# Kernel optimization log

Measured on AMD Instinct MI355X. Metric: run time of the kernel, lower is better.

## Reference

```python
import jax, jax.numpy as jnp
import numpy as np


def _lstm1_step(x, Wih, bih, bhh):
    # nn.LSTM applied to a length-1 sequence with zero initial (h, c):
    # h_prev = 0 so W_hh contributes 0; c = sigmoid(i)*tanh(g); h = sigmoid(o)*tanh(c).
    gates = x @ Wih.T + bih + bhh            # (..., 4H), torch gate order i,f,g,o
    i, f, g, o = jnp.split(gates, 4, axis=-1)
    c = jax.nn.sigmoid(i) * jnp.tanh(g)
    return jax.nn.sigmoid(o) * jnp.tanh(c)


def _lstm2_layer(x, Wih, Whh, bih, bhh):
    # Full recurrent LSTM layer over time; x: (B, T, H) -> outputs (B, T, H).
    B = x.shape[0]
    H = Whh.shape[1]
    xg = x @ Wih.T + bih + bhh               # precompute input gates (B, T, 4H)
    def step(carry, g_t):                    # g_t: (B, 4H)
        h, c = carry
        gates = g_t + h @ Whh.T
        i, f, g, o = jnp.split(gates, 4, axis=-1)
        c = jax.nn.sigmoid(f) * c + jax.nn.sigmoid(i) * jnp.tanh(g)
        h = jax.nn.sigmoid(o) * jnp.tanh(c)
        return (h, c), h
    h0 = jnp.zeros((B, H), x.dtype)
    _, hs = jax.lax.scan(step, (h0, h0), jnp.swapaxes(xg, 0, 1))
    return jnp.swapaxes(hs, 0, 1)            # (B, T, H)


def setup_inputs() -> dict:
    D, H, B, T = 256, 1024, 64, 256
    key = jax.random.key(0)
    ks = iter(jax.random.split(key, 32))
    s = 1.0 / np.sqrt(H).astype(np.float32)
    def u(shape):
        return jax.random.uniform(next(ks), shape, jnp.float32, -s, s)
    inp = {"xx": jax.random.normal(next(ks), (B, T, D), jnp.float32)}
    inp.update(
        l1_Wih0=u((4 * H, D)), l1_bih0=u((4 * H,)), l1_bhh0=u((4 * H,)),
        l1_Wih1=u((4 * H, H)), l1_bih1=u((4 * H,)), l1_bhh1=u((4 * H,)),
        l2_Wih0=u((4 * H, H)), l2_Whh0=u((4 * H, H)), l2_bih0=u((4 * H,)), l2_bhh0=u((4 * H,)),
        l2_Wih1=u((4 * H, H)), l2_Whh1=u((4 * H, H)), l2_bih1=u((4 * H,)), l2_bhh1=u((4 * H,)),
        mlp_W1=u((H, H)), mlp_b1=u((H,)),
        mlp_W2=u((H // 2, H)), mlp_b2=u((H // 2,)),
        mlp_W3=u((1, H // 2)), mlp_b3=u((1,)),
    )
    return inp


def reference(xx, l1_Wih0, l1_bih0, l1_bhh0, l1_Wih1, l1_bih1, l1_bhh1,
              l2_Wih0, l2_Whh0, l2_bih0, l2_bhh0, l2_Wih1, l2_Whh1, l2_bih1, l2_bhh1,
              mlp_W1, mlp_b1, mlp_W2, mlp_b2, mlp_W3, mlp_b3):
    # lstm1: per-timestep single-step stacked LSTM cell with zero state (vectorized over B,T)
    h = _lstm1_step(xx, l1_Wih0, l1_bih0, l1_bhh0)
    h = _lstm1_step(h, l1_Wih1, l1_bih1, l1_bhh1)          # (B, T, H) == lsout
    # lstm2: true 2-layer recurrence over T
    h = _lstm2_layer(h, l2_Wih0, l2_Whh0, l2_bih0, l2_bhh0)
    h = _lstm2_layer(h, l2_Wih1, l2_Whh1, l2_bih1, l2_bhh1)
    last = h[:, -1, :]                                     # (B, H)
    z = jax.nn.relu(last @ mlp_W1.T + mlp_b1)
    z = jax.nn.relu(z @ mlp_W2.T + mlp_b2)
    out = z @ mlp_W3.T + mlp_b3                            # (B, 1)
    return out[:, 0]                                       # out_m: (B,)
```

## Files before the change

### kernel.cpp

```cpp
#include <hip/hip_runtime.h>

typedef unsigned short u16;
typedef unsigned int u32;
typedef u16 u16x8 __attribute__((ext_vector_type(8)));
typedef u16 u16x4 __attribute__((ext_vector_type(4)));
typedef __bf16 bf16x8 __attribute__((ext_vector_type(8)));
typedef float f32x4 __attribute__((ext_vector_type(4)));

#define B_ 64
#define T_ 256
#define D_ 256
#define H_ 1024
#define G4 4096
#define TC 64
#define MC 4096
#define NCHUNK 4
#define NFLG 2048

__device__ __forceinline__ u16 f2bf(float x) {
  u32 u = __builtin_bit_cast(u32, x);
  u += 0x7fffu + ((u >> 16) & 1u);
  return (u16)(u >> 16);
}
__device__ __forceinline__ float bf2f(u16 h) {
  u32 u = ((u32)h) << 16;
  return __builtin_bit_cast(float, u);
}
__device__ __forceinline__ float sigmoidf_(float x) { return 1.f / (1.f + __expf(-x)); }

__device__ __forceinline__ f32x4 mfma16(u16x8 a, u16x8 b, f32x4 c) {
  return __builtin_amdgcn_mfma_f32_16x16x32_bf16(
      __builtin_bit_cast(bf16x8, a), __builtin_bit_cast(bf16x8, b), c, 0, 0, 0);
}

__device__ __forceinline__ void gl2lds16(const u16* g, u16* l) {
  __builtin_amdgcn_global_load_lds(
      (const __attribute__((address_space(1))) u32*)(const void*)g,
      (__attribute__((address_space(3))) u32*)(void*)l, 16, 0, 0);
}

__device__ __forceinline__ void store4_cc(u16* p, u32 v) {
  asm volatile("global_store_dword %0, %1, off sc0 sc1" :: "v"(p), "v"(v) : "memory");
}
__device__ __forceinline__ void store4_cc_u32(u32* p, u32 v) {
  asm volatile("global_store_dword %0, %1, off sc0 sc1" :: "v"(p), "v"(v) : "memory");
}
__device__ __forceinline__ void waitcnt0() {
  asm volatile("s_waitcnt vmcnt(0)" ::: "memory");
}

__global__ void k_split(const float* __restrict__ src, u16* __restrict__ hi,
                        u16* __restrict__ lo, int n4) {
  int i = blockIdx.x * 256 + threadIdx.x;
  if (i >= n4) return;
  const float4* s4 = (const float4*)src;
  float4 v = s4[i];
  u16 h0 = f2bf(v.x), h1 = f2bf(v.y), h2 = f2bf(v.z), h3 = f2bf(v.w);
  u16x4 hv = {h0, h1, h2, h3};
  u16x4 lv = {f2bf(v.x - bf2f(h0)), f2bf(v.y - bf2f(h1)),
              f2bf(v.z - bf2f(h2)), f2bf(v.w - bf2f(h3))};
  *(u16x4*)(hi + 4 * (size_t)i) = hv;
  *(u16x4*)(lo + 4 * (size_t)i) = lv;
}

__global__ void k_split_x(const float* __restrict__ xx, u16* __restrict__ hi,
                          u16* __restrict__ lo, int t0) {
  int i = blockIdx.x * 256 + threadIdx.x;
  if (i >= MC * (D_ / 4)) return;
  int row = i >> 6, c4 = i & 63;
  int b = row >> 6, tc = row & 63;
  const float4* s4 = (const float4*)xx;
  float4 v = s4[(size_t)(b * T_ + t0 + tc) * (D_ / 4) + c4];
  u16 h0 = f2bf(v.x), h1 = f2bf(v.y), h2 = f2bf(v.z), h3 = f2bf(v.w);
  u16x4 hv = {h0, h1, h2, h3};
  u16x4 lv = {f2bf(v.x - bf2f(h0)), f2bf(v.y - bf2f(h1)),
              f2bf(v.z - bf2f(h2)), f2bf(v.w - bf2f(h3))};
  *(u16x4*)(hi + 4 * (size_t)i) = hv;
  *(u16x4*)(lo + 4 * (size_t)i) = lv;
}

__global__ void k_addvec(const float* __restrict__ a, const float* __restrict__ b,
                         float* __restrict__ o, int n) {
  int i = blockIdx.x * 256 + threadIdx.x;
  if (i < n) o[i] = a[i] + b[i];
}

__global__ __launch_bounds__(256, 2) void k_gemm3(
    const u16* __restrict__ Ah, const u16* __restrict__ Al,
    const u16* __restrict__ Bh, const u16* __restrict__ Bl,
    const float* __restrict__ bias, float* __restrict__ C,
    int M, int N, int K, int rec)
{
  __shared__ __attribute__((aligned(16))) u16 sAh[2][4096];
  __shared__ __attribute__((aligned(16))) u16 sAl[2][4096];
  __shared__ __attribute__((aligned(16))) u16 sBh[2][4096];
  __shared__ __attribute__((aligned(16))) u16 sBl[2][4096];

  const int tid = threadIdx.x;
  const int lane = tid & 63;
  const int wv = tid >> 6;
  const int wm = wv & 1, wn = wv >> 1;
  const int m0 = blockIdx.x * 128;
  const int n0 = blockIdx.y * 128;

  const int r0 = tid >> 2;
  const int kg = (tid & 3) ^ (r0 & 3);
  const size_t aoff0 = (size_t)(m0 + r0) * K + kg * 8;
  const size_t aoff1 = (size_t)(m0 + r0 + 64) * K + kg * 8;
  const size_t boff0 = (size_t)(n0 + r0) * K + kg * 8;
  const size_t boff1 = (size_t)(n0 + r0 + 64) * K + kg * 8;
  const int lb0 = wv * 512;
  const int lb1 = 2048 + wv * 512;

  const int l15 = lane & 15, l4 = lane >> 4;
  int afo[4], bfo[4];
#pragma unroll
  for (int mt = 0; mt < 4; ++mt) {
    int r = wm * 64 + mt * 16 + l15;
    afo[mt] = (r * 4 + (l4 ^ (r & 3))) * 8;
  }
#pragma unroll
  for (int nt = 0; nt < 4; ++nt) {
    int r = wn * 64 + nt * 16 + l15;
    bfo[nt] = (r * 4 + (l4 ^ (r & 3))) * 8;
  }

#define STAGE_G(bi, kk) do { \
    gl2lds16(Ah + aoff0 + (kk), &sAh[bi][lb0]); \
    gl2lds16(Ah + aoff1 + (kk), &sAh[bi][lb1]); \
    gl2lds16(Al + aoff0 + (kk), &sAl[bi][lb0]); \
    gl2lds16(Al + aoff1 + (kk), &sAl[bi][lb1]); \
    gl2lds16(Bh + boff0 + (kk), &sBh[bi][lb0]); \
    gl2lds16(Bh + boff1 + (kk), &sBh[bi][lb1]); \
    gl2lds16(Bl + boff0 + (kk), &sBl[bi][lb0]); \
    gl2lds16(Bl + boff1 + (kk), &sBl[bi][lb1]); \
  } while (0)

  f32x4 acc[4][4] = {};

  STAGE_G(0, 0);
  __syncthreads();

  int cur = 0;
  for (int k0 = 0; k0 < K; k0 += 32) {
    if (k0 + 32 < K) STAGE_G(cur ^ 1, k0 + 32);

    u16x8 a_h[4], a_l[4], b_h[4], b_l[4];
#pragma unroll
    for (int i = 0; i < 4; ++i) {
      a_h[i] = *(const u16x8*)&sAh[cur][afo[i]];
      a_l[i] = *(const u16x8*)&sAl[cur][afo[i]];
      b_h[i] = *(const u16x8*)&sBh[cur][bfo[i]];
      b_l[i] = *(const u16x8*)&sBl[cur][bfo[i]];
    }
#pragma unroll
    for (int mt = 0; mt < 4; ++mt)
#pragma unroll
      for (int nt = 0; nt < 4; ++nt) {
        acc[mt][nt] = mfma16(a_h[mt], b_h[nt], acc[mt][nt]);
        acc[mt][nt] = mfma16(a_l[mt], b_h[nt], acc[mt][nt]);
        acc[mt][nt] = mfma16(a_h[mt], b_l[nt], acc[mt][nt]);
      }

    __syncthreads();
    cur ^= 1;
  }
#undef STAGE_G

  if (!rec) {
#pragma unroll
    for (int mt = 0; mt < 4; ++mt) {
      int mr = m0 + wm * 64 + mt * 16 + l4 * 4;
#pragma unroll
      for (int nt = 0; nt < 4; ++nt) {
        int nc = n0 + wn * 64 + nt * 16 + l15;
        float bv = bias[nc];
#pragma unroll
        for (int r = 0; r < 4; ++r)
          C[(size_t)(mr + r) * N + nc] = acc[mt][nt][r] + bv;
      }
    }
  } else {
#pragma unroll
    for (int mt = 0; mt < 4; ++mt) {
      int mr = m0 + wm * 64 + mt * 16 + l4 * 4;
#pragma unroll
      for (int nt = 0; nt < 4; ++nt) {
        int nc = n0 + wn * 64 + nt * 16 + l15;
        float bv = bias[nc];
        int unit = nc & 1023;
        int ublk = unit >> 3;
        int uu = unit & 7;
        int gate = nc >> 10;
#pragma unroll
        for (int r = 0; r < 4; ++r) {
          int m = mr + r;
          int tq = (rec == 1) ? (m & 63) : (m >> 6);
          int bq = (rec == 1) ? (m >> 6) : (m & 63);
          size_t idx = ((size_t)(ublk * 64 + tq) * 4 + gate) * 512 + bq * 8 + uu;
          C[idx] = acc[mt][nt][r] + bv;
        }
      }
    }
  }
}

__global__ void k_pw(const float* __restrict__ xg, u16* __restrict__ hhi,
                     u16* __restrict__ hlo) {
  int idx = blockIdx.x * 256 + threadIdx.x;
  int r = idx >> 10, j = idx & 1023;
  const float* g = xg + (size_t)r * G4;
  float cc = sigmoidf_(g[j]) * tanhf(g[2048 + j]);
  float h = sigmoidf_(g[3072 + j]) * tanhf(cc);
  u16 hh = f2bf(h);
  hhi[idx] = hh;
  hlo[idx] = f2bf(h - bf2f(hh));
}

__global__ __launch_bounds__(512, 2) void k_recd(
    const float* __restrict__ xgA, const float* __restrict__ xgB,
    const u16* __restrict__ WAhi, const u16* __restrict__ WAlo,
    const u16* __restrict__ WBhi, const u16* __restrict__ WBlo,
    u16* __restrict__ rAH, u16* __restrict__ rAL,
    u16* __restrict__ rBH, u16* __restrict__ rBL,
    u16* __restrict__ cAH, u16* __restrict__ cAL,
    u16* __restrict__ cBH, u16* __restrict__ cBL,
    float* __restrict__ cbA, float* __restrict__ cbB,
    float* __restrict__ hfB,
    u32* __restrict__ flags)
{
  __shared__ __attribute__((aligned(16))) u16 sW[66048];
  __shared__ float sg[2][64][34];
  __shared__ int sDead;

  const int tid = threadIdx.x;
  const int lane = tid & 63, wv = tid >> 6;
  const int l15 = lane & 15, l4 = lane >> 4;
  const int L = blockIdx.x >> 7, ublk = blockIdx.x & 127;
  const int u0 = ublk * 8;

  const float* xg = L ? xgB : xgA;
  if (!xg) return;
  const u16* Whi = L ? WBhi : WAhi;
  const u16* Wlo = L ? WBlo : WAlo;
  u16* ringH = L ? rBH : rAH;
  u16* ringL = L ? rBL : rAL;
  u16* carryH = L ? cBH : cAH;
  u16* carryL = L ? cBL : cAL;
  float* cbp = L ? cbB : cbA;
  float* hfinal = L ? hfB : nullptr;
  u32* flg = flags + L * 1024;

  if (tid == 0) sDead = 0;

  for (int ci = tid; ci < 8192; ci += 512) {
    int plane = ci >> 12, rem = ci & 4095;
    int n = rem >> 7, ch = rem & 127;
    int wrow = (n >> 3) * 1024 + u0 + (n & 7);
    const u16* src = (plane ? Wlo : Whi) + (size_t)wrow * 1024 + ch * 8;
    *(u16x8*)&sW[plane * 33024 + n * 1032 + ch * 8] = *(const u16x8*)src;
  }
  __syncthreads();

  const int mt = wv >> 1, kh = wv & 1;
  const int aoff = (mt * 16 + l15) * 1024 + kh * 512 + l4 * 8;
  const int bof0 = l15 * 1032 + kh * 512 + l4 * 8;
  const int bof1 = (16 + l15) * 1032 + kh * 512 + l4 * 8;

  const u32* f0a = flg + (2 * mt) * 128 + kh * 64 + lane;
  const u32* f0b = flg + (2 * mt + 1) * 128 + kh * 64 + lane;
  u32* fown = flg + wv * 128 + ublk;

  const int pb = tid >> 3, uu = tid & 7;
  const int cidx = pb * 1024 + u0 + uu;
  float c = cbp[cidx];
  const float* xgb = xg + (size_t)ublk * 131072 + pb * 8 + uu;

  for (int t = 0; t < TC; ++t) {
    float px0, px1, px2, px3;
    {
      const float* xa = xgb + (size_t)t * 2048;
      asm volatile("global_load_dword %0, %1, off" : "=v"(px0) : "v"(xa));
      asm volatile("global_load_dword %0, %1, off" : "=v"(px1) : "v"(xa + 512));
      asm volatile("global_load_dword %0, %1, off" : "=v"(px2) : "v"(xa + 1024));
      asm volatile("global_load_dword %0, %1, off" : "=v"(px3) : "v"(xa + 1536));
    }

    if (t > 0 && *(volatile int*)&sDead == 0) {
      int guard = 0;
      for (;;) {
        u32 a = __hip_atomic_load(f0a, __ATOMIC_RELAXED, __HIP_MEMORY_SCOPE_AGENT);
        u32 b = __hip_atomic_load(f0b, __ATOMIC_RELAXED, __HIP_MEMORY_SCOPE_AGENT);
        if (a >= (u32)t && b >= (u32)t) break;
        if (++guard > (1 << 17)) { if (lane == 0) sDead = 1; break; }
        __builtin_amdgcn_s_sleep(1);
      }
    }

    const u16* oah = (t ? ringH + (size_t)(t - 1) * 65536 : carryH) + aoff;
    const u16* oal = (t ? ringL + (size_t)(t - 1) * 65536 : carryL) + aoff;
    f32x4 aq[2][2] = {};
#pragma unroll
    for (int kc = 0; kc < 16; ++kc) {
      const int ko = kc * 32;
      u16x8 oh = *(const u16x8*)(oah + ko);
      u16x8 ol = *(const u16x8*)(oal + ko);
      u16x8 b0h = *(const u16x8*)&sW[bof0 + ko];
      u16x8 b0l = *(const u16x8*)&sW[33024 + bof0 + ko];
      u16x8 b1h = *(const u16x8*)&sW[bof1 + ko];
      u16x8 b1l = *(const u16x8*)&sW[33024 + bof1 + ko];
      aq[0][kc & 1] = mfma16(oh, b0h, aq[0][kc & 1]);
      aq[0][kc & 1] = mfma16(ol, b0h, aq[0][kc & 1]);
      aq[0][kc & 1] = mfma16(oh, b0l, aq[0][kc & 1]);
      aq[1][kc & 1] = mfma16(oh, b1h, aq[1][kc & 1]);
      aq[1][kc & 1] = mfma16(ol, b1h, aq[1][kc & 1]);
      aq[1][kc & 1] = mfma16(oh, b1l, aq[1][kc & 1]);
    }
    f32x4 A0 = aq[0][0] + aq[0][1];
    f32x4 A1 = aq[1][0] + aq[1][1];

    __syncthreads();
#pragma unroll
    for (int r4 = 0; r4 < 4; ++r4) {
      int m = mt * 16 + l4 * 4 + r4;
      sg[kh][m][l15] = A0[r4];
      sg[kh][m][16 + l15] = A1[r4];
    }
    __syncthreads();

    float g0 = sg[0][pb][uu] + sg[1][pb][uu];
    float g1 = sg[0][pb][8 + uu] + sg[1][pb][8 + uu];
    float g2 = sg[0][pb][16 + uu] + sg[1][pb][16 + uu];
    float g3 = sg[0][pb][24 + uu] + sg[1][pb][24 + uu];
    waitcnt0();
    g0 += px0; g1 += px1; g2 += px2; g3 += px3;
    c = sigmoidf_(g1) * c + sigmoidf_(g0) * tanhf(g2);
    float h = sigmoidf_(g3) * tanhf(c);
    u32 hiu = (u32)f2bf(h);
    u32 lou = (u32)f2bf(h - bf2f((u16)hiu));
    u32 hiN = __shfl_down(hiu, 1);
    u32 loN = __shfl_down(lou, 1);
    if ((tid & 1) == 0) {
      size_t re = (size_t)t * 65536 + (size_t)pb * 1024 + u0 + uu;
      store4_cc(ringH + re, hiu | (hiN << 16));
      store4_cc(ringL + re, lou | (loN << 16));
      if (t == TC - 1) {
        store4_cc(carryH + cidx, hiu | (hiN << 16));
        store4_cc(carryL + cidx, lou | (loN << 16));
      }
    }
    if (hfinal && t == TC - 1) hfinal[cidx] = h;

    waitcnt0();
    if (lane == 0) store4_cc_u32(fown, (u32)(t + 1));
  }

  cbp[cidx] = c;
}

__global__ void k_fc(const float* __restrict__ in, const float* __restrict__ W,
                     const float* __restrict__ bias, float* __restrict__ out,
                     int K, int N, int relu) {
  int b = blockIdx.x;
  int n = blockIdx.y * 256 + threadIdx.x;
  if (n >= N) return;
  const float4* wr = (const float4*)(W + (size_t)n * K);
  const float4* xr = (const float4*)(in + (size_t)b * K);
  float s = 0.f;
  for (int k = 0; k < K / 4; ++k) {
    float4 w = wr[k], x = xr[k];
    s += w.x * x.x + w.y * x.y + w.z * x.z + w.w * x.w;
  }
  s += bias[n];
  if (relu) s = fmaxf(s, 0.f);
  out[(size_t)b * N + n] = s;
}

__global__ void k_out(const float* __restrict__ z, const float* __restrict__ W3,
                      const float* __restrict__ b3, float* __restrict__ outp) {
  int b = blockIdx.x;
  int lane = threadIdx.x;
  const float4* wr = (const float4*)W3;
  const float4* xr = (const float4*)(z + b * 512);
  float s = 0.f;
  for (int k = lane; k < 128; k += 64) {
    float4 w = wr[k], x = xr[k];
    s += w.x * x.x + w.y * x.y + w.z * x.z + w.w * x.w;
  }
  for (int off = 32; off; off >>= 1) s += __shfl_down(s, off);
  if (lane == 0) outp[b] = s + b3[0];
}

extern "C" void kernel_launch(void* const* d_in, const int* in_sizes, int n_in,
                              void* d_out, int out_size, void* d_ws, size_t ws_size,
                              hipStream_t stream) {
  (void)in_sizes; (void)n_in; (void)out_size; (void)ws_size;
  const float* xx  = (const float*)d_in[0];
  const float* W10 = (const float*)d_in[1];
  const float* b10i = (const float*)d_in[2];
  const float* b10h = (const float*)d_in[3];
  const float* W11 = (const float*)d_in[4];
  const float* b11i = (const float*)d_in[5];
  const float* b11h = (const float*)d_in[6];
  const float* W20 = (const float*)d_in[7];
  const float* Wh0 = (const float*)d_in[8];
  const float* b20i = (const float*)d_in[9];
  const float* b20h = (const float*)d_in[10];
  const float* W21 = (const float*)d_in[11];
  const float* Wh1 = (const float*)d_in[12];
  const float* b21i = (const float*)d_in[13];
  const float* b21h = (const float*)d_in[14];
  const float* mW1 = (const float*)d_in[15];
  const float* mb1 = (const float*)d_in[16];
  const float* mW2 = (const float*)d_in[17];
  const float* mb2 = (const float*)d_in[18];
  const float* mW3 = (const float*)d_in[19];
  const float* mb3 = (const float*)d_in[20];

  char* ws = (char*)d_ws;
  size_t o = 0;
  float* XG0 = (float*)(ws + o); o += (size_t)MC * G4 * 4;
  float* XG1 = (float*)(ws + o); o += (size_t)MC * G4 * 4;
  u16* Aah = (u16*)(ws + o); o += (size_t)MC * H_ * 2;
  u16* Aal = (u16*)(ws + o); o += (size_t)MC * H_ * 2;
  u16* Abh = (u16*)(ws + o); o += (size_t)MC * H_ * 2;
  u16* Abl = (u16*)(ws + o); o += (size_t)MC * H_ * 2;
  u16* XXh = (u16*)(ws + o); o += (size_t)MC * D_ * 2;
  u16* XXl = (u16*)(ws + o); o += (size_t)MC * D_ * 2;
  u16* W10h = (u16*)(ws + o); o += (size_t)G4 * D_ * 2;
  u16* W10l = (u16*)(ws + o); o += (size_t)G4 * D_ * 2;
  u16* W11h = (u16*)(ws + o); o += (size_t)G4 * H_ * 2;
  u16* W11l = (u16*)(ws + o); o += (size_t)G4 * H_ * 2;
  u16* W20h = (u16*)(ws + o); o += (size_t)G4 * H_ * 2;
  u16* W20l = (u16*)(ws + o); o += (size_t)G4 * H_ * 2;
  u16* Wh0h = (u16*)(ws + o); o += (size_t)G4 * H_ * 2;
  u16* Wh0l = (u16*)(ws + o); o += (size_t)G4 * H_ * 2;
  u16* W21h = (u16*)(ws + o); o += (size_t)G4 * H_ * 2;
  u16* W21l = (u16*)(ws + o); o += (size_t)G4 * H_ * 2;
  u16* Wh1h = (u16*)(ws + o); o += (size_t)G4 * H_ * 2;
  u16* Wh1l = (u16*)(ws + o); o += (size_t)G4 * H_ * 2;
  float* bs0 = (float*)(ws + o); o += G4 * 4;
  float* bs1 = (float*)(ws + o); o += G4 * 4;
  float* bs2 = (float*)(ws + o); o += G4 * 4;
  float* bs3 = (float*)(ws + o); o += G4 * 4;
  char* ST = ws + o;
  u16* h00H = (u16*)(ws + o); o += B_ * H_ * 2;
  u16* h00L = (u16*)(ws + o); o += B_ * H_ * 2;
  u16* h01H = (u16*)(ws + o); o += B_ * H_ * 2;
  u16* h01L = (u16*)(ws + o); o += B_ * H_ * 2;
  float* cb0 = (float*)(ws + o); o += B_ * H_ * 4;
  float* cb1 = (float*)(ws + o); o += B_ * H_ * 4;
  u32* FLG = (u32*)(ws + o); o += (NCHUNK + 1) * NFLG * 4;
  size_t stBytes = (size_t)((ws + o) - ST);
  float* FH = (float*)(ws + o); o += B_ * H_ * 4;
  float* Z1 = (float*)(ws + o); o += B_ * H_ * 4;
  float* Z2 = (float*)(ws + o); o += B_ * 512 * 4;

  u16 *r0H = Abh, *r0L = Abl, *r1H = Aah, *r1L = Aal;

  k_split<<<(G4 * D_ / 4 + 255) / 256, 256, 0, stream>>>(W10, W10h, W10l, G4 * D_ / 4);
  k_split<<<(G4 * H_ / 4 + 255) / 256, 256, 0, stream>>>(W11, W11h, W11l, G4 * H_ / 4);
  k_split<<<(G4 * H_ / 4 + 255) / 256, 256, 0, stream>>>(W20, W20h, W20l, G4 * H_ / 4);
  k_split<<<(G4 * H_ / 4 + 255) / 256, 256, 0, stream>>>(Wh0, Wh0h, Wh0l, G4 * H_ / 4);
  k_split<<<(G4 * H_ / 4 + 255) / 256, 256, 0, stream>>>(W21, W21h, W21l, G4 * H_ / 4);
  k_split<<<(G4 * H_ / 4 + 255) / 256, 256, 0, stream>>>(Wh1, Wh1h, Wh1l, G4 * H_ / 4);
  k_addvec<<<16, 256, 0, stream>>>(b10i, b10h, bs0, G4);
  k_addvec<<<16, 256, 0, stream>>>(b11i, b11h, bs1, G4);
  k_addvec<<<16, 256, 0, stream>>>(b20i, b20h, bs2, G4);
  k_addvec<<<16, 256, 0, stream>>>(b21i, b21h, bs3, G4);
  hipMemsetAsync(ST, 0, stBytes, stream);

  dim3 gg(MC / 128, G4 / 128);
  const int pwBlocks = MC * H_ / 256;

  for (int c = 0; c < NCHUNK; ++c) {
    int t0 = c * TC;
    k_split_x<<<(MC * (D_ / 4) + 255) / 256, 256, 0, stream>>>(xx, XXh, XXl, t0);
    k_gemm3<<<gg, 256, 0, stream>>>(XXh, XXl, W10h, W10l, bs0, XG0, MC, G4, D_, 0);
    k_pw<<<pwBlocks, 256, 0, stream>>>(XG0, Aah, Aal);
    k_gemm3<<<gg, 256, 0, stream>>>(Aah, Aal, W11h, W11l, bs1, XG0, MC, G4, H_, 0);
    k_pw<<<pwBlocks, 256, 0, stream>>>(XG0, Abh, Abl);
    k_gemm3<<<gg, 256, 0, stream>>>(Abh, Abl, W20h, W20l, bs2, XG0, MC, G4, H_, 1);
    k_recd<<<256, 512, 0, stream>>>(XG0, (c > 0) ? XG1 : nullptr,
                                    Wh0h, Wh0l, Wh1h, Wh1l,
                                    r0H, r0L, r1H, r1L,
                                    h00H, h00L, h01H, h01L, cb0, cb1,
                                    nullptr, FLG + c * NFLG);
    k_gemm3<<<gg, 256, 0, stream>>>(r0H, r0L, W21h, W21l, bs3, XG1, MC, G4, H_, 2);
  }
  k_recd<<<256, 512, 0, stream>>>(nullptr, XG1,
                                  Wh0h, Wh0l, Wh1h, Wh1l,
                                  r0H, r0L, r1H, r1L,
                                  h00H, h00L, h01H, h01L, cb0, cb1,
                                  FH, FLG + NCHUNK * NFLG);

  k_fc<<<dim3(B_, 4), 256, 0, stream>>>(FH, mW1, mb1, Z1, H_, H_, 1);
  k_fc<<<dim3(B_, 2), 256, 0, stream>>>(Z1, mW2, mb2, Z2, H_, 512, 1);
  k_out<<<B_, 64, 0, stream>>>(Z2, mW3, mb3, (float*)d_out);
}
```

Before: 4.729 ms.

## Fuse LSTM1 pointwise into GEMM epilogue via gate-permuted weights; halve chunk size

The first-stage weight rows and biases are permuted so that each 64-column GEMM tile holds the i, f, g and o gates for the same 16 hidden units. A new epilogue mode then computes the zero-state LSTM cell directly and writes the split bf16 hidden state. This removes both k_pw kernels and the full fp32 gate round-trip through memory for lstm1. Separately, the time chunk shrinks from 64 to 32 steps (8 chunks), which means more kernel launches and more recurrent-kernel weight reloads in exchange for smaller intermediate buffers.

```diff
diff --git a/kernel.cpp b/kernel.cpp
--- a/kernel.cpp
+++ b/kernel.cpp
@@ -12,9 +12,10 @@
 #define D_ 256
 #define H_ 1024
 #define G4 4096
-#define TC 64
-#define MC 4096
-#define NCHUNK 4
+#define TC 32
+#define TCSH 5
+#define MC 2048
+#define NCHUNK 8
 #define NFLG 2048
 
 __device__ __forceinline__ u16 f2bf(float x) {
@@ -63,12 +64,30 @@
   *(u16x4*)(lo + 4 * (size_t)i) = lv;
 }
 
+__global__ void k_splitp(const float* __restrict__ src, u16* __restrict__ hi,
+                         u16* __restrict__ lo, int n4, int s) {
+  int i = blockIdx.x * 256 + threadIdx.x;
+  if (i >= n4) return;
+  int row = i >> s, col4 = i & ((1 << s) - 1);
+  int g = row >> 10, u = row & 1023;
+  int prow = ((u >> 4) << 6) + (g << 4) + (u & 15);
+  size_t di = ((size_t)prow << s) | col4;
+  const float4* s4 = (const float4*)src;
+  float4 v = s4[i];
+  u16 h0 = f2bf(v.x), h1 = f2bf(v.y), h2 = f2bf(v.z), h3 = f2bf(v.w);
+  u16x4 hv = {h0, h1, h2, h3};
+  u16x4 lv = {f2bf(v.x - bf2f(h0)), f2bf(v.y - bf2f(h1)),
+              f2bf(v.z - bf2f(h2)), f2bf(v.w - bf2f(h3))};
+  *(u16x4*)(hi + 4 * di) = hv;
+  *(u16x4*)(lo + 4 * di) = lv;
+}
+
 __global__ void k_split_x(const float* __restrict__ xx, u16* __restrict__ hi,
                           u16* __restrict__ lo, int t0) {
   int i = blockIdx.x * 256 + threadIdx.x;
   if (i >= MC * (D_ / 4)) return;
   int row = i >> 6, c4 = i & 63;
-  int b = row >> 6, tc = row & 63;
+  int b = row >> TCSH, tc = row & (TC - 1);
   const float4* s4 = (const float4*)xx;
   float4 v = s4[(size_t)(b * T_ + t0 + tc) * (D_ / 4) + c4];
   u16 h0 = f2bf(v.x), h1 = f2bf(v.y), h2 = f2bf(v.z), h3 = f2bf(v.w);
@@ -85,10 +104,20 @@
   if (i < n) o[i] = a[i] + b[i];
 }
 
+__global__ void k_addp(const float* __restrict__ a, const float* __restrict__ b,
+                       float* __restrict__ o) {
+  int i = blockIdx.x * 256 + threadIdx.x;
+  if (i >= G4) return;
+  int g = i >> 10, u = i & 1023;
+  int prow = ((u >> 4) << 6) + (g << 4) + (u & 15);
+  o[prow] = a[i] + b[i];
+}
+
 __global__ __launch_bounds__(256, 2) void k_gemm3(
     const u16* __restrict__ Ah, const u16* __restrict__ Al,
     const u16* __restrict__ Bh, const u16* __restrict__ Bl,
     const float* __restrict__ bias, float* __restrict__ C,
+    u16* __restrict__ Hh, u16* __restrict__ Hl,
     int M, int N, int K, int rec)
 {
   __shared__ __attribute__((aligned(16))) u16 sAh[2][4096];
@@ -167,7 +196,7 @@
   }
 #undef STAGE_G
 
-  if (!rec) {
+  if (rec == 0) {
 #pragma unroll
     for (int mt = 0; mt < 4; ++mt) {
       int mr = m0 + wm * 64 + mt * 16 + l4 * 4;
@@ -178,6 +207,28 @@
 #pragma unroll
         for (int r = 0; r < 4; ++r)
           C[(size_t)(mr + r) * N + nc] = acc[mt][nt][r] + bv;
+      }
+    }
+  } else if (rec == 3) {
+    const int cb = n0 + wn * 64;
+    const int ub = (cb >> 6) * 16 + l15;
+    const float bvi = bias[cb + l15];
+    const float bvg = bias[cb + 32 + l15];
+    const float bvo = bias[cb + 48 + l15];
+#pragma unroll
+    for (int mt = 0; mt < 4; ++mt) {
+      int mr = m0 + wm * 64 + mt * 16 + l4 * 4;
+#pragma unroll
+      for (int r = 0; r < 4; ++r) {
+        float gi = acc[mt][0][r] + bvi;
+        float gg = acc[mt][2][r] + bvg;
+        float go = acc[mt][3][r] + bvo;
+        float cc2 = sigmoidf_(gi) * tanhf(gg);
+        float h = sigmoidf_(go) * tanhf(cc2);
+        u16 hh = f2bf(h);
+        size_t oi = (size_t)(mr + r) * 1024 + ub;
+        Hh[oi] = hh;
+        Hl[oi] = f2bf(h - bf2f(hh));
       }
     }
   } else {
@@ -195,26 +246,14 @@
 #pragma unroll
         for (int r = 0; r < 4; ++r) {
           int m = mr + r;
-          int tq = (rec == 1) ? (m & 63) : (m >> 6);
-          int bq = (rec == 1) ? (m >> 6) : (m & 63);
-          size_t idx = ((size_t)(ublk * 64 + tq) * 4 + gate) * 512 + bq * 8 + uu;
+          int tq = (rec == 1) ? (m & (TC - 1)) : (m >> 6);
+          int bq = (rec == 1) ? (m >> TCSH) : (m & 63);
+          size_t idx = ((size_t)(ublk * TC + tq) * 4 + gate) * 512 + bq * 8 + uu;
           C[idx] = acc[mt][nt][r] + bv;
         }
       }
     }
   }
-}
-
-__global__ void k_pw(const float* __restrict__ xg, u16* __restrict__ hhi,
-                     u16* __restrict__ hlo) {
-  int idx = blockIdx.x * 256 + threadIdx.x;
-  int r = idx >> 10, j = idx & 1023;
-  const float* g = xg + (size_t)r * G4;
-  float cc = sigmoidf_(g[j]) * tanhf(g[2048 + j]);
-  float h = sigmoidf_(g[3072 + j]) * tanhf(cc);
-  u16 hh = f2bf(h);
-  hhi[idx] = hh;
-  hlo[idx] = f2bf(h - bf2f(hh));
 }
 
 __global__ __launch_bounds__(512, 2) void k_recd(
@@ -274,7 +313,7 @@
   const int pb = tid >> 3, uu = tid & 7;
   const int cidx = pb * 1024 + u0 + uu;
   float c = cbp[cidx];
-  const float* xgb = xg + (size_t)ublk * 131072 + pb * 8 + uu;
+  const float* xgb = xg + (size_t)ublk * (TC * 2048) + pb * 8 + uu;
 
   for (int t = 0; t < TC; ++t) {
     float px0, px1, px2, px3;
@@ -458,35 +497,36 @@
 
   u16 *r0H = Abh, *r0L = Abl, *r1H = Aah, *r1L = Aal;
 
-  k_split<<<(G4 * D_ / 4 + 255) / 256, 256, 0, stream>>>(W10, W10h, W10l, G4 * D_ / 4);
-  k_split<<<(G4 * H_ / 4 + 255) / 256, 256, 0, stream>>>(W11, W11h, W11l, G4 * H_ / 4);
+  k_splitp<<<(G4 * D_ / 4 + 255) / 256, 256, 0, stream>>>(W10, W10h, W10l, G4 * D_ / 4, 6);
+  k_splitp<<<(G4 * H_ / 4 + 255) / 256, 256, 0, stream>>>(W11, W11h, W11l, G4 * H_ / 4, 8);
   k_split<<<(G4 * H_ / 4 + 255) / 256, 256, 0, stream>>>(W20, W20h, W20l, G4 * H_ / 4);
   k_split<<<(G4 * H_ / 4 + 255) / 256, 256, 0, stream>>>(Wh0, Wh0h, Wh0l, G4 * H_ / 4);
   k_split<<<(G4 * H_ / 4 + 255) / 256, 256, 0, stream>>>(W21, W21h, W21l, G4 * H_ / 4);
   k_split<<<(G4 * H_ / 4 + 255) / 256, 256, 0, stream>>>(Wh1, Wh1h, Wh1l, G4 * H_ / 4);
-  k_addvec<<<16, 256, 0, stream>>>(b10i, b10h, bs0, G4);
-  k_addvec<<<16, 256, 0, stream>>>(b11i, b11h, bs1, G4);
+  k_addp<<<16, 256, 0, stream>>>(b10i, b10h, bs0);
+  k_addp<<<16, 256, 0, stream>>>(b11i, b11h, bs1);
   k_addvec<<<16, 256, 0, stream>>>(b20i, b20h, bs2, G4);
   k_addvec<<<16, 256, 0, stream>>>(b21i, b21h, bs3, G4);
   hipMemsetAsync(ST, 0, stBytes, stream);
 
   dim3 gg(MC / 128, G4 / 128);
-  const int pwBlocks = MC * H_ / 256;
 
   for (int c = 0; c < NCHUNK; ++c) {
     int t0 = c * TC;
     k_split_x<<<(MC * (D_ / 4) + 255) / 256, 256, 0, stream>>>(xx, XXh, XXl, t0);
-    k_gemm3<<<gg, 256, 0, stream>>>(XXh, XXl, W10h, W10l, bs0, XG0, MC, G4, D_, 0);
-    k_pw<<<pwBlocks, 256, 0, stream>>>(XG0, Aah, Aal);
-    k_gemm3<<<gg, 256, 0, stream>>>(Aah, Aal, W11h, W11l, bs1, XG0, MC, G4, H_, 0);
-    k_pw<<<pwBlocks, 256, 0, stream>>>(XG0, Abh, Abl);
-    k_gemm3<<<gg, 256, 0, stream>>>(Abh, Abl, W20h, W20l, bs2, XG0, MC, G4, H_, 1);
+    k_gemm3<<<gg, 256, 0, stream>>>(XXh, XXl, W10h, W10l, bs0, nullptr,
+                                    Aah, Aal, MC, G4, D_, 3);
+    k_gemm3<<<gg, 256, 0, stream>>>(Aah, Aal, W11h, W11l, bs1, nullptr,
+                                    Abh, Abl, MC, G4, H_, 3);
+    k_gemm3<<<gg, 256, 0, stream>>>(Abh, Abl, W20h, W20l, bs2, XG0,
+                                    nullptr, nullptr, MC, G4, H_, 1);
     k_recd<<<256, 512, 0, stream>>>(XG0, (c > 0) ? XG1 : nullptr,
                                     Wh0h, Wh0l, Wh1h, Wh1l,
                                     r0H, r0L, r1H, r1L,
                                     h00H, h00L, h01H, h01L, cb0, cb1,
                                     nullptr, FLG + c * NFLG);
-    k_gemm3<<<gg, 256, 0, stream>>>(r0H, r0L, W21h, W21l, bs3, XG1, MC, G4, H_, 2);
+    k_gemm3<<<gg, 256, 0, stream>>>(r0H, r0L, W21h, W21l, bs3, XG1,
+                                    nullptr, nullptr, MC, G4, H_, 2);
   }
   k_recd<<<256, 512, 0, stream>>>(nullptr, XG1,
                                   Wh0h, Wh0l, Wh1h, Wh1l,
```

Result: faster. 4.518 ms (-4.5%).
